# Kernel tuning notes

Hardware: AMD Instinct MI355X
Metric: run time of the kernel (lower is better)

Reference implementation:

```python
import jax, jax.numpy as jnp
import numpy as np

B, T, C = 8, 4096, 512


def setup_inputs() -> dict:
    key = jax.random.key(0)
    k1, k2, k3 = jax.random.split(key, 3)
    inputs = jax.random.normal(k1, (B, T, C), dtype=jnp.float32)
    # stable-ish recurrence: |A| < 1
    A_real = jax.random.uniform(k2, (C,), dtype=jnp.float32, minval=0.5, maxval=0.99)
    A_imag = jax.random.uniform(k3, (C,), dtype=jnp.float32, minval=-0.1, maxval=0.1)
    h0_real = jnp.zeros((B, C), dtype=jnp.float32)
    h0_imag = jnp.zeros((B, C), dtype=jnp.float32)
    return {"inputs": inputs, "A_real": A_real, "A_imag": A_imag,
            "h0_real": h0_real, "h0_imag": h0_imag}


def reference(inputs, A_real, A_imag, h0_real, h0_imag):
    # Diagonal complex linear recurrence:
    #   h[t] = A * h[t-1] + x[t]   (x real, added to real part only)
    # Output: states at every step, stacked (real, imag) -> (B, T, C, 2)
    def step(carry, x_t):
        hr, hi = carry
        nr = hr * A_real - hi * A_imag + x_t
        ni = A_imag * hr + A_real * hi
        return (nr, ni), (nr, ni)

    xs = jnp.swapaxes(inputs, 0, 1)  # (T, B, C)
    _, (real_seq, imag_seq) = jax.lax.scan(step, (h0_real, h0_imag), xs)
    real_seq = jnp.swapaxes(real_seq, 0, 1)  # (B, T, C)
    imag_seq = jnp.swapaxes(imag_seq, 0, 1)
    return jnp.stack([real_seq, imag_seq], axis=-1)  # (B, T, C, 2)
```

## Files before the change

kernel.cpp:

```cpp
#include <hip/hip_runtime.h>

#define BB 8
#define TT 4096
#define CC 512
#define NCHUNK 128
#define LCHUNK (TT / NCHUNK)

__global__ __launch_bounds__(256, 4) void rec_ends(const float* __restrict__ x,
                                                   const float* __restrict__ Ar,
                                                   const float* __restrict__ Ai,
                                                   float4* __restrict__ s_end) {
    const int tid   = threadIdx.x;
    const int blk   = blockIdx.x;
    const int b     = blk / NCHUNK;
    const int chunk = blk % NCHUNK;
    const int t0    = chunk * LCHUNK;

    const float2 a_r = ((const float2*)Ar)[tid];
    const float2 a_i = ((const float2*)Ai)[tid];

    const float2* xp = (const float2*)(x + (size_t)(b * TT + t0) * CC) + tid;

    float hr0 = 0.f, hi0 = 0.f, hr1 = 0.f, hi1 = 0.f;
#pragma unroll 8
    for (int t = 0; t < LCHUNK; ++t) {
        float2 xv = xp[(size_t)t * (CC / 2)];
        float nr0 = fmaf(hr0, a_r.x, fmaf(-hi0, a_i.x, xv.x));
        float ni0 = fmaf(a_i.x, hr0, a_r.x * hi0);
        float nr1 = fmaf(hr1, a_r.y, fmaf(-hi1, a_i.y, xv.y));
        float ni1 = fmaf(a_i.y, hr1, a_r.y * hi1);
        hr0 = nr0; hi0 = ni0; hr1 = nr1; hi1 = ni1;
    }
    s_end[(size_t)(chunk * BB + b) * (CC / 2) + tid] = make_float4(hr0, hi0, hr1, hi1);
}

__global__ __launch_bounds__(256, 4) void rec_emit(const float* __restrict__ x,
                                                   const float* __restrict__ Ar,
                                                   const float* __restrict__ Ai,
                                                   const float* __restrict__ h0r,
                                                   const float* __restrict__ h0i,
                                                   const float4* __restrict__ s_end,
                                                   float4* __restrict__ out) {
    const int tid   = threadIdx.x;
    const int blk   = blockIdx.x;
    const int b     = blk / NCHUNK;
    const int chunk = blk % NCHUNK;
    const int t0    = chunk * LCHUNK;

    const float2 a_r = ((const float2*)Ar)[tid];
    const float2 a_i = ((const float2*)Ai)[tid];

    float p0r = a_r.x, p0i = a_i.x, p1r = a_r.y, p1i = a_i.y;
#pragma unroll
    for (int s = 0; s < 5; ++s) {
        float n0r = p0r * p0r - p0i * p0i, n0i = 2.f * p0r * p0i;
        float n1r = p1r * p1r - p1i * p1i, n1i = 2.f * p1r * p1i;
        p0r = n0r; p0i = n0i; p1r = n1r; p1i = n1i;
    }

    float2 h0rv = ((const float2*)(h0r + (size_t)b * CC))[tid];
    float2 h0iv = ((const float2*)(h0i + (size_t)b * CC))[tid];
    float hr0 = h0rv.x, hr1 = h0rv.y, hi0 = h0iv.x, hi1 = h0iv.y;

    const float4* sp = s_end + tid;
#pragma unroll 4
    for (int j = 0; j < chunk; ++j) {
        float4 s = sp[(size_t)(j * BB + b) * (CC / 2)];
        float nr0 = p0r * hr0 - p0i * hi0 + s.x;
        float ni0 = p0i * hr0 + p0r * hi0 + s.y;
        float nr1 = p1r * hr1 - p1i * hi1 + s.z;
        float ni1 = p1i * hr1 + p1r * hi1 + s.w;
        hr0 = nr0; hi0 = ni0; hr1 = nr1; hi1 = ni1;
    }

    const float2* xp = (const float2*)(x + (size_t)(b * TT + t0) * CC) + tid;
    float4* op = out + (size_t)(b * TT + t0) * (CC / 2) + tid;
#pragma unroll 8
    for (int t = 0; t < LCHUNK; ++t) {
        float2 xv = xp[(size_t)t * (CC / 2)];
        float nr0 = fmaf(hr0, a_r.x, fmaf(-hi0, a_i.x, xv.x));
        float ni0 = fmaf(a_i.x, hr0, a_r.x * hi0);
        float nr1 = fmaf(hr1, a_r.y, fmaf(-hi1, a_i.y, xv.y));
        float ni1 = fmaf(a_i.y, hr1, a_r.y * hi1);
        hr0 = nr0; hi0 = ni0; hr1 = nr1; hi1 = ni1;
        op[(size_t)t * (CC / 2)] = make_float4(nr0, ni0, nr1, ni1);
    }
}

extern "C" void kernel_launch(void* const* d_in, const int* in_sizes, int n_in,
                              void* d_out, int out_size, void* d_ws, size_t ws_size,
                              hipStream_t stream) {
    const float* x   = (const float*)d_in[0];
    const float* Ar  = (const float*)d_in[1];
    const float* Ai  = (const float*)d_in[2];
    const float* h0r = (const float*)d_in[3];
    const float* h0i = (const float*)d_in[4];
    float* out = (float*)d_out;

    float4* s_end = (float4*)d_ws;

    rec_ends<<<BB * NCHUNK, 256, 0, stream>>>(x, Ar, Ai, s_end);
    rec_emit<<<BB * NCHUNK, 256, 0, stream>>>(x, Ar, Ai, h0r, h0i, s_end, (float4*)out);
}
```

Measured before the change: 207.0 us.

## Fuse chunk-scan passes into one cooperative kernel with grid sync

Merges the chunk-end pass and the emit pass into one cooperative kernel separated by a grid-wide sync. Each thread keeps its chunk of x in registers, so the input is read from memory once instead of twice, and one kernel launch is removed. Outputs are written with nontemporal stores. In exchange it adds grid-sync latency and more register pressure, and it depends on all 1024 blocks being co-resident; if the cooperative launch fails it falls back to the original two kernels.

```diff
diff --git a/kernel.cpp b/kernel.cpp
--- a/kernel.cpp
+++ b/kernel.cpp
@@ -1,10 +1,89 @@
 #include <hip/hip_runtime.h>
+#include <hip/hip_cooperative_groups.h>
+
+namespace cg = cooperative_groups;
 
 #define BB 8
 #define TT 4096
 #define CC 512
 #define NCHUNK 128
 #define LCHUNK (TT / NCHUNK)
+
+typedef float floatx4 __attribute__((ext_vector_type(4)));
+
+__global__ __launch_bounds__(256, 4) void rec_fused(const float* __restrict__ x,
+                                                    const float* __restrict__ Ar,
+                                                    const float* __restrict__ Ai,
+                                                    const float* __restrict__ h0r,
+                                                    const float* __restrict__ h0i,
+                                                    float4* __restrict__ s_end,
+                                                    float4* __restrict__ out) {
+    const int tid   = threadIdx.x;
+    const int blk   = blockIdx.x;
+    const int b     = blk / NCHUNK;
+    const int chunk = blk % NCHUNK;
+    const int t0    = chunk * LCHUNK;
+
+    const float2 a_r = ((const float2*)Ar)[tid];
+    const float2 a_i = ((const float2*)Ai)[tid];
+
+    const float2* xp = (const float2*)(x + (size_t)(b * TT + t0) * CC) + tid;
+
+    float2 xs[LCHUNK];
+#pragma unroll
+    for (int t = 0; t < LCHUNK; ++t)
+        xs[t] = xp[(size_t)t * (CC / 2)];
+
+    float hr0 = 0.f, hi0 = 0.f, hr1 = 0.f, hi1 = 0.f;
+#pragma unroll
+    for (int t = 0; t < LCHUNK; ++t) {
+        float2 xv = xs[t];
+        float nr0 = fmaf(hr0, a_r.x, fmaf(-hi0, a_i.x, xv.x));
+        float ni0 = fmaf(a_i.x, hr0, a_r.x * hi0);
+        float nr1 = fmaf(hr1, a_r.y, fmaf(-hi1, a_i.y, xv.y));
+        float ni1 = fmaf(a_i.y, hr1, a_r.y * hi1);
+        hr0 = nr0; hi0 = ni0; hr1 = nr1; hi1 = ni1;
+    }
+    s_end[(size_t)(chunk * BB + b) * (CC / 2) + tid] = make_float4(hr0, hi0, hr1, hi1);
+
+    cg::this_grid().sync();
+
+    float p0r = a_r.x, p0i = a_i.x, p1r = a_r.y, p1i = a_i.y;
+#pragma unroll
+    for (int s = 0; s < 5; ++s) {
+        float n0r = p0r * p0r - p0i * p0i, n0i = 2.f * p0r * p0i;
+        float n1r = p1r * p1r - p1i * p1i, n1i = 2.f * p1r * p1i;
+        p0r = n0r; p0i = n0i; p1r = n1r; p1i = n1i;
+    }
+
+    float2 h0rv = ((const float2*)(h0r + (size_t)b * CC))[tid];
+    float2 h0iv = ((const float2*)(h0i + (size_t)b * CC))[tid];
+    hr0 = h0rv.x; hr1 = h0rv.y; hi0 = h0iv.x; hi1 = h0iv.y;
+
+    const float4* sp = s_end + tid;
+#pragma unroll 4
+    for (int j = 0; j < chunk; ++j) {
+        float4 s = sp[(size_t)(j * BB + b) * (CC / 2)];
+        float nr0 = p0r * hr0 - p0i * hi0 + s.x;
+        float ni0 = p0i * hr0 + p0r * hi0 + s.y;
+        float nr1 = p1r * hr1 - p1i * hi1 + s.z;
+        float ni1 = p1i * hr1 + p1r * hi1 + s.w;
+        hr0 = nr0; hi0 = ni0; hr1 = nr1; hi1 = ni1;
+    }
+
+    floatx4* op = (floatx4*)(out + (size_t)(b * TT + t0) * (CC / 2) + tid);
+#pragma unroll
+    for (int t = 0; t < LCHUNK; ++t) {
+        float2 xv = xs[t];
+        float nr0 = fmaf(hr0, a_r.x, fmaf(-hi0, a_i.x, xv.x));
+        float ni0 = fmaf(a_i.x, hr0, a_r.x * hi0);
+        float nr1 = fmaf(hr1, a_r.y, fmaf(-hi1, a_i.y, xv.y));
+        float ni1 = fmaf(a_i.y, hr1, a_r.y * hi1);
+        hr0 = nr0; hi0 = ni0; hr1 = nr1; hi1 = ni1;
+        floatx4 v = {nr0, ni0, nr1, ni1};
+        __builtin_nontemporal_store(v, &op[(size_t)t * (CC / 2)]);
+    }
+}
 
 __global__ __launch_bounds__(256, 4) void rec_ends(const float* __restrict__ x,
                                                    const float* __restrict__ Ar,
@@ -18,7 +97,6 @@
 
     const float2 a_r = ((const float2*)Ar)[tid];
     const float2 a_i = ((const float2*)Ai)[tid];
-
     const float2* xp = (const float2*)(x + (size_t)(b * TT + t0) * CC) + tid;
 
     float hr0 = 0.f, hi0 = 0.f, hr1 = 0.f, hi1 = 0.f;
@@ -95,10 +173,16 @@
     const float* Ai  = (const float*)d_in[2];
     const float* h0r = (const float*)d_in[3];
     const float* h0i = (const float*)d_in[4];
-    float* out = (float*)d_out;
+    float4* s_end = (float4*)d_ws;
+    float4* outp  = (float4*)d_out;
 
-    float4* s_end = (float4*)d_ws;
-
-    rec_ends<<<BB * NCHUNK, 256, 0, stream>>>(x, Ar, Ai, s_end);
-    rec_emit<<<BB * NCHUNK, 256, 0, stream>>>(x, Ar, Ai, h0r, h0i, s_end, (float4*)out);
+    void* args[] = {(void*)&x, (void*)&Ar, (void*)&Ai, (void*)&h0r,
+                    (void*)&h0i, (void*)&s_end, (void*)&outp};
+    hipError_t err = hipLaunchCooperativeKernel((const void*)rec_fused,
+                                                dim3(BB * NCHUNK), dim3(256),
+                                                args, 0, stream);
+    if (err != hipSuccess) {
+        rec_ends<<<BB * NCHUNK, 256, 0, stream>>>(x, Ar, Ai, s_end);
+        rec_emit<<<BB * NCHUNK, 256, 0, stream>>>(x, Ar, Ai, h0r, h0i, s_end, outp);
+    }
 }
```

After: 313.0 us. 1.51x slower.

## Fuse chunk-end and emit passes into one kernel with flag-based lookback

Applied to the files above, without the earlier changes.

Merges the two-pass chunked scan into a single kernel. Each block caches its chunk of x in registers, publishes its chunk-end state with a release flag, then spins on the flags of earlier chunks before combining their states and emitting outputs with nontemporal stores. This avoids reading x twice and removes one launch. In exchange it relies on earlier blocks being scheduled first to avoid deadlock. The flags use a fixed magic value and are never reset between calls, so stale flags from a previous run could let a later call read old chunk states.

```diff
diff --git a/kernel.cpp b/kernel.cpp
--- a/kernel.cpp
+++ b/kernel.cpp
@@ -5,11 +5,18 @@
 #define CC 512
 #define NCHUNK 128
 #define LCHUNK (TT / NCHUNK)
+#define FLAG_MAGIC 0x1337BEEFu
 
-__global__ __launch_bounds__(256, 4) void rec_ends(const float* __restrict__ x,
-                                                   const float* __restrict__ Ar,
-                                                   const float* __restrict__ Ai,
-                                                   float4* __restrict__ s_end) {
+typedef float floatx4 __attribute__((ext_vector_type(4)));
+
+__global__ __launch_bounds__(256, 4) void rec_lookback(const float* __restrict__ x,
+                                                       const float* __restrict__ Ar,
+                                                       const float* __restrict__ Ai,
+                                                       const float* __restrict__ h0r,
+                                                       const float* __restrict__ h0i,
+                                                       float4* __restrict__ s_end,
+                                                       unsigned int* __restrict__ flags,
+                                                       float4* __restrict__ out) {
     const int tid   = threadIdx.x;
     const int blk   = blockIdx.x;
     const int b     = blk / NCHUNK;
@@ -18,37 +25,33 @@
 
     const float2 a_r = ((const float2*)Ar)[tid];
     const float2 a_i = ((const float2*)Ai)[tid];
+    const float2 h0rv = ((const float2*)(h0r + (size_t)b * CC))[tid];
+    const float2 h0iv = ((const float2*)(h0i + (size_t)b * CC))[tid];
 
     const float2* xp = (const float2*)(x + (size_t)(b * TT + t0) * CC) + tid;
 
+    float2 xs[LCHUNK];
+#pragma unroll
+    for (int t = 0; t < LCHUNK; ++t)
+        xs[t] = xp[(size_t)t * (CC / 2)];
+
     float hr0 = 0.f, hi0 = 0.f, hr1 = 0.f, hi1 = 0.f;
-#pragma unroll 8
+#pragma unroll
     for (int t = 0; t < LCHUNK; ++t) {
-        float2 xv = xp[(size_t)t * (CC / 2)];
+        float2 xv = xs[t];
         float nr0 = fmaf(hr0, a_r.x, fmaf(-hi0, a_i.x, xv.x));
         float ni0 = fmaf(a_i.x, hr0, a_r.x * hi0);
         float nr1 = fmaf(hr1, a_r.y, fmaf(-hi1, a_i.y, xv.y));
         float ni1 = fmaf(a_i.y, hr1, a_r.y * hi1);
         hr0 = nr0; hi0 = ni0; hr1 = nr1; hi1 = ni1;
     }
+
     s_end[(size_t)(chunk * BB + b) * (CC / 2) + tid] = make_float4(hr0, hi0, hr1, hi1);
-}
-
-__global__ __launch_bounds__(256, 4) void rec_emit(const float* __restrict__ x,
-                                                   const float* __restrict__ Ar,
-                                                   const float* __restrict__ Ai,
-                                                   const float* __restrict__ h0r,
-                                                   const float* __restrict__ h0i,
-                                                   const float4* __restrict__ s_end,
-                                                   float4* __restrict__ out) {
-    const int tid   = threadIdx.x;
-    const int blk   = blockIdx.x;
-    const int b     = blk / NCHUNK;
-    const int chunk = blk % NCHUNK;
-    const int t0    = chunk * LCHUNK;
-
-    const float2 a_r = ((const float2*)Ar)[tid];
-    const float2 a_i = ((const float2*)Ai)[tid];
+    __threadfence();
+    __syncthreads();
+    if (tid == 0)
+        __hip_atomic_store(&flags[b * NCHUNK + chunk], FLAG_MAGIC,
+                           __ATOMIC_RELEASE, __HIP_MEMORY_SCOPE_AGENT);
 
     float p0r = a_r.x, p0i = a_i.x, p1r = a_r.y, p1i = a_i.y;
 #pragma unroll
@@ -58,10 +61,14 @@
         p0r = n0r; p0i = n0i; p1r = n1r; p1i = n1i;
     }
 
-    float2 h0rv = ((const float2*)(h0r + (size_t)b * CC))[tid];
-    float2 h0iv = ((const float2*)(h0i + (size_t)b * CC))[tid];
-    float hr0 = h0rv.x, hr1 = h0rv.y, hi0 = h0iv.x, hi1 = h0iv.y;
+    if (tid < chunk) {
+        while (__hip_atomic_load(&flags[b * NCHUNK + tid], __ATOMIC_RELAXED,
+                                 __HIP_MEMORY_SCOPE_AGENT) != FLAG_MAGIC) {}
+    }
+    __syncthreads();
+    __builtin_amdgcn_fence(__ATOMIC_ACQUIRE, "agent");
 
+    hr0 = h0rv.x; hr1 = h0rv.y; hi0 = h0iv.x; hi1 = h0iv.y;
     const float4* sp = s_end + tid;
 #pragma unroll 4
     for (int j = 0; j < chunk; ++j) {
@@ -73,17 +80,17 @@
         hr0 = nr0; hi0 = ni0; hr1 = nr1; hi1 = ni1;
     }
 
-    const float2* xp = (const float2*)(x + (size_t)(b * TT + t0) * CC) + tid;
-    float4* op = out + (size_t)(b * TT + t0) * (CC / 2) + tid;
-#pragma unroll 8
+    floatx4* op = (floatx4*)(out + (size_t)(b * TT + t0) * (CC / 2) + tid);
+#pragma unroll
     for (int t = 0; t < LCHUNK; ++t) {
-        float2 xv = xp[(size_t)t * (CC / 2)];
+        float2 xv = xs[t];
         float nr0 = fmaf(hr0, a_r.x, fmaf(-hi0, a_i.x, xv.x));
         float ni0 = fmaf(a_i.x, hr0, a_r.x * hi0);
         float nr1 = fmaf(hr1, a_r.y, fmaf(-hi1, a_i.y, xv.y));
         float ni1 = fmaf(a_i.y, hr1, a_r.y * hi1);
         hr0 = nr0; hi0 = ni0; hr1 = nr1; hi1 = ni1;
-        op[(size_t)t * (CC / 2)] = make_float4(nr0, ni0, nr1, ni1);
+        floatx4 v = {nr0, ni0, nr1, ni1};
+        __builtin_nontemporal_store(v, &op[(size_t)t * (CC / 2)]);
     }
 }
 
@@ -95,10 +102,10 @@
     const float* Ai  = (const float*)d_in[2];
     const float* h0r = (const float*)d_in[3];
     const float* h0i = (const float*)d_in[4];
-    float* out = (float*)d_out;
 
     float4* s_end = (float4*)d_ws;
+    unsigned int* flags = (unsigned int*)((char*)d_ws + (size_t)NCHUNK * BB * (CC / 2) * 16);
 
-    rec_ends<<<BB * NCHUNK, 256, 0, stream>>>(x, Ar, Ai, s_end);
-    rec_emit<<<BB * NCHUNK, 256, 0, stream>>>(x, Ar, Ai, h0r, h0i, s_end, (float4*)out);
+    rec_lookback<<<BB * NCHUNK, 256, 0, stream>>>(x, Ar, Ai, h0r, h0i,
+                                                  s_end, flags, (float4*)d_out);
 }
```

Result: slower. 403.1 us (+94.7%).
